# Optimization experiments

Hardware: AMD Instinct MI355X
Metric: run time of the kernel (lower is better)

## Reference

```python
import jax, jax.numpy as jnp
import numpy as np

N_HEADS = 16


def _rope(q, k, freq_cos, freq_sin):
    # q,k: [B,S,H,hd]; freqs: [S, hd//2]
    B, S, H, hd = q.shape
    qr, qi = q.reshape(B, S, H, hd // 2, 2)[..., 0], q.reshape(B, S, H, hd // 2, 2)[..., 1]
    kr, ki = k.reshape(B, S, H, hd // 2, 2)[..., 0], k.reshape(B, S, H, hd // 2, 2)[..., 1]
    fc = freq_cos[None, :, None, :]  # [1,S,1,hd//2]
    fs = freq_sin[None, :, None, :]
    q_out = jnp.stack([qr * fc - qi * fs, qr * fs + qi * fc], axis=-1).reshape(B, S, H, hd)
    k_out = jnp.stack([kr * fc - ki * fs, kr * fs + ki * fc], axis=-1).reshape(B, S, H, hd)
    return q_out, k_out


def setup_inputs() -> dict:
    key = jax.random.key(0)
    ks = jax.random.split(key, 7)
    B, S, D = 2, 2048, 2048
    hd = D // N_HEADS
    scale = 1.0 / np.sqrt(D)
    return {
        "x": jax.random.normal(ks[0], (B, S, D), dtype=jnp.float32),
        "freq_cos": jnp.cos(jax.random.normal(ks[1], (S, hd // 2), dtype=jnp.float32)),
        "freq_sin": jnp.sin(jax.random.normal(ks[2], (S, hd // 2), dtype=jnp.float32)),
        "wq": jax.random.normal(ks[3], (D, D), dtype=jnp.float32) * scale,
        "wk": jax.random.normal(ks[4], (D, D), dtype=jnp.float32) * scale,
        "wv": jax.random.normal(ks[5], (D, D), dtype=jnp.float32) * scale,
        "wo": jax.random.normal(ks[6], (D, D), dtype=jnp.float32) * scale,
    }


def reference(x, freq_cos, freq_sin, wq, wk, wv, wo):
    B, S, D = x.shape
    H = N_HEADS
    hd = D // H
    # torch nn.Linear(weight [out,in]): y = x @ W^T
    q = (x @ wq.T).reshape(B, S, H, hd)
    k = (x @ wk.T).reshape(B, S, H, hd)
    v = (x @ wv.T).reshape(B, S, H, hd)
    q, k = _rope(q, k, freq_cos, freq_sin)
    # [B,H,S,hd]
    q = q.transpose(0, 2, 1, 3)
    k = k.transpose(0, 2, 1, 3)
    v = v.transpose(0, 2, 1, 3)
    scores = jnp.einsum("bhqd,bhkd->bhqk", q, k) / jnp.sqrt(jnp.float32(hd))
    causal = jnp.triu(jnp.full((S, S), -jnp.inf, dtype=scores.dtype), k=1)
    scores = scores + causal[None, None, :, :]
    probs = jax.nn.softmax(scores, axis=-1)
    out = jnp.einsum("bhqk,bhkd->bhqd", probs, v)
    out = out.transpose(0, 2, 1, 3).reshape(B, S, D)
    return out @ wo.T
```

## Files before the change

kernel.cpp:

```cpp
#include <hip/hip_runtime.h>
#include <hip/hip_bf16.h>
#include <stdint.h>

typedef unsigned short u16;
typedef unsigned int   u32;

typedef __attribute__((ext_vector_type(8))) short bf16x8;
typedef __attribute__((ext_vector_type(4))) float f32x4;
typedef __attribute__((ext_vector_type(4))) float f4;
typedef __attribute__((ext_vector_type(4))) u16   u16x4;

#define GLOBAL_AS __attribute__((address_space(1)))
#define LDS_AS    __attribute__((address_space(3)))

#define QSCALE (0.088388347648318447f * 1.4426950408889634f)

__device__ __forceinline__ void gload_lds16(const void* gsrc, void* ldst) {
    __builtin_amdgcn_global_load_lds((GLOBAL_AS const u32*)gsrc,
                                     (LDS_AS u32*)ldst, 16, 0, 0);
}

__device__ __forceinline__ float b2f(u16 u) {
    union { u32 i; float f; } x; x.i = ((u32)u) << 16; return x.f;
}
__device__ __forceinline__ u16 f2b(float f) {
    u32 u = __builtin_bit_cast(u32, f);
    u = (u + 0x7fff + ((u >> 16) & 1)) >> 16;
    return (u16)u;
}
__device__ __forceinline__ u16 f2b_tr(float f) {
    return (u16)(__builtin_bit_cast(u32, f) >> 16);
}

__global__ __launch_bounds__(256) void f2bf_kernel(const float* __restrict__ in,
                                                   u16* __restrict__ out, int n4) {
    int i = blockIdx.x * blockDim.x + threadIdx.x;
    if (i >= n4) return;
    f4 v = ((const f4*)in)[i];
    u16x4 o;
    o[0] = f2b(v[0]); o[1] = f2b(v[1]); o[2] = f2b(v[2]); o[3] = f2b(v[3]);
    ((u16x4*)out)[i] = o;
}

__global__ __launch_bounds__(256) void rope_kernel(u16* __restrict__ qkv,
                                                   const float* __restrict__ fc,
                                                   const float* __restrict__ fs) {
    const int S = 2048;
    int idx = blockIdx.x * blockDim.x + threadIdx.x;
    const int p   = idx & 1023;
    const int row = idx >> 10;
    const int s   = row & (S - 1);
    const int i   = p & 63;
    const float c = fc[s * 64 + i], sn = fs[s * 64 + i];
    u16* qa = qkv + (size_t)row * 6144 + p * 2;
    u16* ka = qa + 2048;
    u32 qq = *(const u32*)qa;
    float qr = b2f((u16)(qq & 0xffff)), qi = b2f((u16)(qq >> 16));
    u32 kk = *(const u32*)ka;
    float kr = b2f((u16)(kk & 0xffff)), ki = b2f((u16)(kk >> 16));
    u16 e0 = f2b(qr * c - qi * sn), e1 = f2b(qr * sn + qi * c);
    *(u32*)qa = (u32)e0 | ((u32)e1 << 16);
    e0 = f2b(kr * c - ki * sn); e1 = f2b(kr * sn + ki * c);
    *(u32*)ka = (u32)e0 | ((u32)e1 << 16);
}

#define BARR() do { asm volatile("" ::: "memory"); \
                    __builtin_amdgcn_s_barrier();  \
                    asm volatile("" ::: "memory"); } while (0)

template<int OUT_MODE>
__global__ __launch_bounds__(512, 2)
void gemm8(const u16* __restrict__ A, const u16* __restrict__ B,
           void* __restrict__ Cptr, int M, int N, int Kdim) {
    __shared__ char lds[131072];
    const int t = threadIdx.x, l = t & 63, w = t >> 6;
    const int g = l >> 4, r16 = l & 15;
    const int wm = w >> 2, wn = w & 3;

    const int nwg = gridDim.x * gridDim.y;
    const int id  = blockIdx.y * gridDim.x + blockIdx.x;
    const int swz = (id & 7) * (nwg >> 3) + (id >> 3);
    const int bx  = swz % gridDim.x, by = swz / gridDim.x;
    const int m0 = by * 256, n0 = bx * 256;

    f32x4 acc[8][4];
#pragma unroll
    for (int i = 0; i < 8; i++)
#pragma unroll
        for (int j = 0; j < 4; j++) acc[i][j] = (f32x4){0.f, 0.f, 0.f, 0.f};

    const int sw  = (r16 & 7) << 4;
    const int cK0 = (g * 16) ^ sw;
    const int cK1 = (64 + g * 16) ^ sw;

    bf16x8 afA[4][2], bfA[2][2], bfB[2][2];

    auto stgA = [&](int d, int r, int kt) {
#pragma unroll
        for (int i = 0; i < 2; i++) {
            const int o  = (i * 8 + w) * 1024 + l * 16;
            const int rr = o >> 7;
            const int cb = (o & 127) ^ ((rr & 7) << 4);
            const int gr = ((rr >> 6) << 7) + r * 64 + (rr & 63);
            gload_lds16(A + (size_t)(m0 + gr) * Kdim + kt * 64 + (cb >> 1),
                        lds + d * 65536 + r * 16384 + (i * 8 + w) * 1024);
        }
    };
    auto stgB = [&](int d, int r, int kt) {
#pragma unroll
        for (int i = 0; i < 2; i++) {
            const int o  = (i * 8 + w) * 1024 + l * 16;
            const int rr = o >> 7;
            const int cb = (o & 127) ^ ((rr & 7) << 4);
            const int gc = ((rr >> 5) << 6) + r * 32 + (rr & 31);
            gload_lds16(B + (size_t)(n0 + gc) * Kdim + kt * 64 + (cb >> 1),
                        lds + d * 65536 + 32768 + r * 16384 + (i * 8 + w) * 1024);
        }
    };
    auto rdA = [&](int d, int qm) {
#pragma unroll
        for (int mi = 0; mi < 4; mi++) {
            const char* p = lds + d * 65536 + qm * 16384
                            + (wm * 64 + mi * 16 + r16) * 128;
            afA[mi][0] = *(const bf16x8*)(p + cK0);
            afA[mi][1] = *(const bf16x8*)(p + cK1);
        }
    };
    auto rdB = [&](bf16x8 (&dst)[2][2], int d, int qn) {
#pragma unroll
        for (int ni = 0; ni < 2; ni++) {
            const char* p = lds + d * 65536 + 32768 + qn * 16384
                            + (wn * 32 + ni * 16 + r16) * 128;
            dst[ni][0] = *(const bf16x8*)(p + cK0);
            dst[ni][1] = *(const bf16x8*)(p + cK1);
        }
    };
    auto mm = [&](int qm, int qn, bf16x8 (&bf)[2][2]) {
        __builtin_amdgcn_s_setprio(1);
#pragma unroll
        for (int kk = 0; kk < 2; kk++)
#pragma unroll
            for (int mi = 0; mi < 4; mi++)
#pragma unroll
                for (int ni = 0; ni < 2; ni++)
                    acc[qm * 4 + mi][qn * 2 + ni] =
                        __builtin_amdgcn_mfma_f32_16x16x32_bf16(
                            afA[mi][kk], bf[ni][kk],
                            acc[qm * 4 + mi][qn * 2 + ni], 0, 0, 0);
        __builtin_amdgcn_s_setprio(0);
    };

    const int nk = Kdim >> 6;

    stgA(0, 0, 0); stgB(0, 1, 0); stgB(0, 0, 0); stgA(0, 1, 0);
    stgA(1, 0, 1); stgB(1, 1, 1);
    asm volatile("s_waitcnt vmcnt(4)" ::: "memory");
    BARR();

    for (int tt = 0; tt < (nk >> 1); ++tt) {
        const int b1 = (2 * tt + 1);
        const int a2 = (2 * tt + 2) & (nk - 1);
        const int b2 = (2 * tt + 3) & (nk - 1);

        rdA(0, 0); rdB(bfA, 0, 0); stgB(1, 0, b1); BARR();
        mm(0, 0, bfA); BARR();
        rdB(bfB, 0, 1); stgA(1, 1, b1); BARR();
        mm(0, 1, bfB); BARR();
        rdA(0, 1); stgA(0, 0, a2); BARR();
        mm(1, 1, bfB); BARR();
        stgB(0, 1, a2); BARR();
        mm(1, 0, bfA);
        asm volatile("s_waitcnt vmcnt(4)" ::: "memory");
        BARR();
        rdA(1, 0); rdB(bfA, 1, 0); stgB(0, 0, a2); BARR();
        mm(0, 0, bfA); BARR();
        rdB(bfB, 1, 1); stgA(0, 1, a2); BARR();
        mm(0, 1, bfB); BARR();
        rdA(1, 1); stgA(1, 0, b2); BARR();
        mm(1, 1, bfB); BARR();
        stgB(1, 1, b2); BARR();
        mm(1, 0, bfA);
        asm volatile("s_waitcnt vmcnt(4)" ::: "memory");
        BARR();
    }

#pragma unroll
    for (int a = 0; a < 8; a++)
#pragma unroll
        for (int b = 0; b < 4; b++)
#pragma unroll
            for (int r = 0; r < 4; r++) {
                int row = m0 + wm * 128 + a * 16 + g * 4 + r;
                int col = n0 + wn * 64 + b * 16 + r16;
                float v = acc[a][b][r];
                if (OUT_MODE == 0)      ((float*)Cptr)[(size_t)row * N + col] = v;
                else if (OUT_MODE == 1) ((u16*)Cptr)[(size_t)row * N + col] = f2b(v);
                else ((u16*)Cptr)[(size_t)row * N + col] =
                         f2b(col < 2048 ? v * QSCALE : v);
            }
}

template<int OUT_MODE>
__global__ __launch_bounds__(512, 2)
void gemm_bt(const u16* __restrict__ A, const u16* __restrict__ B,
             void* __restrict__ Cptr, int M, int N, int Kdim) {
    __shared__ char lds[3][49152];
    const int t = threadIdx.x, l = t & 63, w = t >> 6;
    const int g = l >> 4, r16 = l & 15;

    const int nwg = gridDim.x * gridDim.y;
    const int id  = blockIdx.y * gridDim.x + blockIdx.x;
    const int swz = (id & 7) * (nwg >> 3) + (id >> 3);
    const int bx  = swz % gridDim.x, by = swz / gridDim.x;
    const int m0 = by * 256, n0 = bx * 128;
    const int wm = w >> 1, wn = w & 1;
    const int rA = wm * 64, rB = wn * 64;

    f32x4 acc[4][4];
#pragma unroll
    for (int i = 0; i < 4; i++)
#pragma unroll
        for (int j = 0; j < 4; j++) acc[i][j] = (f32x4){0.f, 0.f, 0.f, 0.f};

    const int nk = Kdim >> 6;

    auto stage = [&](int kt, int bi) {
        const int k0 = kt << 6;
#pragma unroll
        for (int q = 0; q < 4; q++) {
            const int o = q * 8192 + w * 1024 + l * 16;
            const int row = o >> 7;
            const int cb = (o & 127) ^ ((row & 7) << 4);
            gload_lds16(A + (size_t)(m0 + row) * Kdim + k0 + (cb >> 1),
                        &lds[bi][q * 8192 + w * 1024]);
        }
#pragma unroll
        for (int q = 0; q < 2; q++) {
            const int o = q * 8192 + w * 1024 + l * 16;
            const int row = o >> 7;
            const int cb = (o & 127) ^ ((row & 7) << 4);
            gload_lds16(B + (size_t)(n0 + row) * Kdim + k0 + (cb >> 1),
                        &lds[bi][32768 + q * 8192 + w * 1024]);
        }
    };

    stage(0, 0);
    stage(1, 1);

    for (int kt = 0; kt < nk; ++kt) {
        const int cur = kt % 3;
        __builtin_amdgcn_sched_barrier(0);
        __builtin_amdgcn_s_barrier();
        stage((kt + 2) % nk, (kt + 2) % 3);
        asm volatile("s_waitcnt vmcnt(12)" ::: "memory");
        __builtin_amdgcn_s_barrier();
        __builtin_amdgcn_sched_barrier(0);

        const char* Ab = lds[cur];
        const char* Bb = lds[cur] + 32768;
        bf16x8 af[2][4], bfr[2][4];
#pragma unroll
        for (int kk = 0; kk < 2; kk++)
#pragma unroll
            for (int i = 0; i < 4; i++) {
                const int rowa = rA + i * 16 + r16;
                const int cba = (kk * 64 + g * 16) ^ ((rowa & 7) << 4);
                af[kk][i] = *(const bf16x8*)(Ab + rowa * 128 + cba);
                const int rowb = rB + i * 16 + r16;
                const int cbb = (kk * 64 + g * 16) ^ ((rowb & 7) << 4);
                bfr[kk][i] = *(const bf16x8*)(Bb + rowb * 128 + cbb);
            }
#pragma unroll
        for (int kk = 0; kk < 2; kk++)
#pragma unroll
            for (int mi = 0; mi < 4; mi++)
#pragma unroll
                for (int ni = 0; ni < 4; ni++)
                    acc[mi][ni] = __builtin_amdgcn_mfma_f32_16x16x32_bf16(af[kk][mi],
                                                                          bfr[kk][ni],
                                                                          acc[mi][ni], 0, 0, 0);
    }

#pragma unroll
    for (int mi = 0; mi < 4; mi++)
#pragma unroll
        for (int ni = 0; ni < 4; ni++)
#pragma unroll
            for (int r = 0; r < 4; r++) {
                int row = m0 + rA + mi * 16 + g * 4 + r;
                int col = n0 + rB + ni * 16 + r16;
                float v = acc[mi][ni][r];
                if (OUT_MODE == 0)      ((float*)Cptr)[(size_t)row * N + col] = v;
                else if (OUT_MODE == 1) ((u16*)Cptr)[(size_t)row * N + col] = f2b(v);
                else ((u16*)Cptr)[(size_t)row * N + col] =
                         f2b(col < 2048 ? v * QSCALE : v);
            }
}

__global__ __launch_bounds__(512, 2)
void flash_attn(const u16* __restrict__ QKV, u16* __restrict__ Op) {
    const int S = 2048, DQ = 6144, DO = 2048;
    __shared__ u16 klds[2][128 * 128];
    __shared__ u16 vtlds[128 * 136];
    __shared__ u16 plds[8][16 * 136];
    const int t = threadIdx.x, l = t & 63, w = t >> 6;
    const int g = l >> 4, r16 = l & 15;
    const int bh = blockIdx.x, b = bh >> 4, h = bh & 15;
    const size_t base = ((size_t)(b * S)) * DQ + h * 128;
    const u16* qp = QKV + base;
    const u16* kp = qp + 2048;
    const u16* vp = qp + 4096;
    const size_t obase = ((size_t)(b * S)) * DO + h * 128;

    for (int task = 0; task < 2; ++task) {
        const int tq = task ? (15 - (int)blockIdx.y) : (int)blockIdx.y;
        const int q0 = tq * 128;
        const int nkt = tq + 1;

        bf16x8 qf[4];
#pragma unroll
        for (int ks = 0; ks < 4; ks++)
            qf[ks] = *(const bf16x8*)(qp + (size_t)(q0 + w * 16 + r16) * DQ
                                      + ks * 32 + g * 8);

        f32x4 acc[8];
#pragma unroll
        for (int i = 0; i < 8; i++) acc[i] = (f32x4){0.f, 0.f, 0.f, 0.f};
        float m_run[4], s_run[4];
#pragma unroll
        for (int r = 0; r < 4; r++) { m_run[r] = -3.0e38f; s_run[r] = 0.f; }

        auto stageK = [&](int bi, int kv0) {
#pragma unroll
            for (int i = 0; i < 4; i++) {
                const int o = (w * 4 + i) * 1024 + l * 16;
                const int row = o >> 8;
                const int cb = (o & 255) ^ ((row & 7) << 4);
                gload_lds16(kp + (size_t)(kv0 + row) * DQ + (cb >> 1),
                            (char*)klds[bi] + (w * 4 + i) * 1024);
            }
        };
        bf16x8 vv[2][2];
        auto loadV = [&](int kv0) {
#pragma unroll
            for (int c = 0; c < 2; c++)
#pragma unroll
                for (int kh = 0; kh < 2; kh++)
                    vv[c][kh] = *(const bf16x8*)(vp + (size_t)(kv0 + kh * 64 + l) * DQ
                                                 + (w * 16 + c * 8));
        };
        auto writeVT = [&]() {
#pragma unroll
            for (int c = 0; c < 2; c++)
#pragma unroll
                for (int kh = 0; kh < 2; kh++) {
                    const int d0 = w * 16 + c * 8;
#pragma unroll
                    for (int j = 0; j < 8; j++)
                        vtlds[(d0 + j) * 136 + kh * 64 + l] = (u16)vv[c][kh][j];
                }
        };

        stageK(0, 0);
        loadV(0);
        __syncthreads();
        writeVT();
        __syncthreads();

        int cur = 0;
        for (int kt = 0; kt < nkt; ++kt) {
            const int kv0 = kt * 128;
            const bool more = (kt + 1 < nkt);
            if (more) { stageK(cur ^ 1, kv0 + 128); loadV(kv0 + 128); }

            f32x4 sf[8];
#pragma unroll
            for (int nf = 0; nf < 8; nf++) sf[nf] = (f32x4){0.f, 0.f, 0.f, 0.f};
#pragma unroll
            for (int nf = 0; nf < 8; nf++) {
                const int row = nf * 16 + r16;
                const int rb = row * 256;
#pragma unroll
                for (int ks = 0; ks < 4; ks++) {
                    const int cb = (ks * 64 + g * 16) ^ ((row & 7) << 4);
                    bf16x8 kf = *(const bf16x8*)((const char*)klds[cur] + rb + cb);
                    sf[nf] = __builtin_amdgcn_mfma_f32_16x16x32_bf16(qf[ks], kf,
                                                                     sf[nf], 0, 0, 0);
                }
            }

            const bool diag = (kt == tq);
            float mt[4];
#pragma unroll
            for (int r = 0; r < 4; r++) mt[r] = -3.0e38f;
#pragma unroll
            for (int nf = 0; nf < 8; nf++)
#pragma unroll
                for (int r = 0; r < 4; r++) {
                    float s = sf[nf][r];
                    if (diag) {
                        int qrow = q0 + w * 16 + g * 4 + r;
                        int kcol = kv0 + nf * 16 + r16;
                        if (kcol > qrow) s = -3.0e38f;
                    }
                    sf[nf][r] = s;
                    mt[r] = fmaxf(mt[r], s);
                }
#pragma unroll
            for (int r = 0; r < 4; r++) {
#pragma unroll
                for (int d = 1; d < 16; d <<= 1)
                    mt[r] = fmaxf(mt[r], __shfl_xor(mt[r], d));
            }
            int grow = (mt[0] > m_run[0] + 8.f) | (mt[1] > m_run[1] + 8.f) |
                       (mt[2] > m_run[2] + 8.f) | (mt[3] > m_run[3] + 8.f);
            if (__any(grow)) {
#pragma unroll
                for (int r = 0; r < 4; r++) {
                    float mn = fmaxf(m_run[r], mt[r]);
                    float alpha = exp2f(m_run[r] - mn);
                    m_run[r] = mn;
                    s_run[r] *= alpha;
#pragma unroll
                    for (int i = 0; i < 8; i++) acc[i][r] *= alpha;
                }
            }
            float psum[4];
#pragma unroll
            for (int r = 0; r < 4; r++) psum[r] = 0.f;
#pragma unroll
            for (int nf = 0; nf < 8; nf++)
#pragma unroll
                for (int r = 0; r < 4; r++) {
                    float p = exp2f(sf[nf][r] - m_run[r]);
                    psum[r] += p;
                    plds[w][(g * 4 + r) * 136 + nf * 16 + r16] = f2b_tr(p);
                }
#pragma unroll
            for (int r = 0; r < 4; r++) {
#pragma unroll
                for (int d = 1; d < 16; d <<= 1)
                    psum[r] += __shfl_xor(psum[r], d);
                s_run[r] += psum[r];
            }
            __builtin_amdgcn_s_setprio(1);
#pragma unroll
            for (int ks2 = 0; ks2 < 4; ks2++) {
                bf16x8 pf = *(const bf16x8*)(&plds[w][r16 * 136 + ks2 * 32 + g * 8]);
#pragma unroll
                for (int nf8 = 0; nf8 < 8; nf8++) {
                    bf16x8 vf = *(const bf16x8*)(&vtlds[(nf8 * 16 + r16) * 136
                                                         + ks2 * 32 + g * 8]);
                    acc[nf8] = __builtin_amdgcn_mfma_f32_16x16x32_bf16(pf, vf,
                                                                       acc[nf8], 0, 0, 0);
                }
            }
            __builtin_amdgcn_s_setprio(0);

            __syncthreads();
            if (more) writeVT();
            __syncthreads();
            cur ^= 1;
        }

        float inv[4];
#pragma unroll
        for (int r = 0; r < 4; r++) inv[r] = 1.0f / s_run[r];
#pragma unroll
        for (int nf8 = 0; nf8 < 8; nf8++)
#pragma unroll
            for (int r = 0; r < 4; r++) {
                size_t idx = obase + (size_t)(q0 + w * 16 + g * 4 + r) * DO
                             + nf8 * 16 + r16;
                Op[idx] = f2b(acc[nf8][r] * inv[r]);
            }
    }
}

extern "C" void kernel_launch(void* const* d_in, const int* in_sizes, int n_in,
                              void* d_out, int out_size, void* d_ws, size_t ws_size,
                              hipStream_t stream) {
    const float* x  = (const float*)d_in[0];
    const float* fc = (const float*)d_in[1];
    const float* fs = (const float*)d_in[2];
    const float* wq = (const float*)d_in[3];
    const float* wk = (const float*)d_in[4];
    const float* wv = (const float*)d_in[5];
    const float* wo = (const float*)d_in[6];
    float* out = (float*)d_out;

    const int S = 2048, D = 2048;
    const int M = 2 * S;
    const size_t MD = (size_t)M * D;
    const size_t DD = (size_t)D * D;

    u16* xb   = (u16*)d_ws;
    u16* wqb  = xb  + MD;
    u16* wkb  = wqb + DD;
    u16* wvb  = wkb + DD;
    u16* wob  = wvb + DD;
    u16* qkvb = wob + DD;

    f2bf_kernel<<<(int)(MD / 1024), 256, 0, stream>>>(x,  xb,  (int)(MD / 4));
    f2bf_kernel<<<(int)(DD / 1024), 256, 0, stream>>>(wq, wqb, (int)(DD / 4));
    f2bf_kernel<<<(int)(DD / 1024), 256, 0, stream>>>(wk, wkb, (int)(DD / 4));
    f2bf_kernel<<<(int)(DD / 1024), 256, 0, stream>>>(wv, wvb, (int)(DD / 4));
    f2bf_kernel<<<(int)(DD / 1024), 256, 0, stream>>>(wo, wob, (int)(DD / 4));

    gemm8<2><<<dim3(6144 / 256, M / 256), 512, 0, stream>>>(xb, wqb, qkvb, M, 6144, D);

    rope_kernel<<<(int)(MD / 2 / 256), 256, 0, stream>>>(qkvb, fc, fs);

    flash_attn<<<dim3(32, 8), 512, 0, stream>>>(qkvb, xb);

    gemm_bt<0><<<dim3(D / 128, M / 256), 512, 0, stream>>>(xb, wob, out, M, D, D);
}
```

Before: 286.5 us.

## Fuse RoPE into QKV GEMM epilogue and merge fp32-to-bf16 casts

```diff
diff --git a/kernel.cpp b/kernel.cpp
--- a/kernel.cpp
+++ b/kernel.cpp
@@ -32,38 +32,27 @@
     return (u16)(__builtin_bit_cast(u32, f) >> 16);
 }
 
-__global__ __launch_bounds__(256) void f2bf_kernel(const float* __restrict__ in,
-                                                   u16* __restrict__ out, int n4) {
+__global__ __launch_bounds__(256)
+void f2bf_all(const float* __restrict__ x,  const float* __restrict__ wq,
+              const float* __restrict__ wk, const float* __restrict__ wv,
+              const float* __restrict__ wo, u16* __restrict__ out,
+              int md4, int dd4, int n4) {
     int i = blockIdx.x * blockDim.x + threadIdx.x;
     if (i >= n4) return;
-    f4 v = ((const f4*)in)[i];
+    const float* src; int off;
+    if (i < md4) { src = x; off = i; }
+    else {
+        int j = i - md4;
+        int k = j / dd4;
+        off = j - k * dd4;
+        src = (k == 0) ? wq : (k == 1) ? wk : (k == 2) ? wv : wo;
+    }
+    f4 v = ((const f4*)src)[off];
     u16x4 o;
     o[0] = f2b(v[0]); o[1] = f2b(v[1]); o[2] = f2b(v[2]); o[3] = f2b(v[3]);
     ((u16x4*)out)[i] = o;
 }
 
-__global__ __launch_bounds__(256) void rope_kernel(u16* __restrict__ qkv,
-                                                   const float* __restrict__ fc,
-                                                   const float* __restrict__ fs) {
-    const int S = 2048;
-    int idx = blockIdx.x * blockDim.x + threadIdx.x;
-    const int p   = idx & 1023;
-    const int row = idx >> 10;
-    const int s   = row & (S - 1);
-    const int i   = p & 63;
-    const float c = fc[s * 64 + i], sn = fs[s * 64 + i];
-    u16* qa = qkv + (size_t)row * 6144 + p * 2;
-    u16* ka = qa + 2048;
-    u32 qq = *(const u32*)qa;
-    float qr = b2f((u16)(qq & 0xffff)), qi = b2f((u16)(qq >> 16));
-    u32 kk = *(const u32*)ka;
-    float kr = b2f((u16)(kk & 0xffff)), ki = b2f((u16)(kk >> 16));
-    u16 e0 = f2b(qr * c - qi * sn), e1 = f2b(qr * sn + qi * c);
-    *(u32*)qa = (u32)e0 | ((u32)e1 << 16);
-    e0 = f2b(kr * c - ki * sn); e1 = f2b(kr * sn + ki * c);
-    *(u32*)ka = (u32)e0 | ((u32)e1 << 16);
-}
-
 #define BARR() do { asm volatile("" ::: "memory"); \
                     __builtin_amdgcn_s_barrier();  \
                     asm volatile("" ::: "memory"); } while (0)
@@ -71,7 +60,8 @@
 template<int OUT_MODE>
 __global__ __launch_bounds__(512, 2)
 void gemm8(const u16* __restrict__ A, const u16* __restrict__ B,
-           void* __restrict__ Cptr, int M, int N, int Kdim) {
+           void* __restrict__ Cptr, int M, int N, int Kdim,
+           const float* __restrict__ fc, const float* __restrict__ fs) {
     __shared__ char lds[131072];
     const int t = threadIdx.x, l = t & 63, w = t >> 6;
     const int g = l >> 4, r16 = l & 15;
@@ -193,10 +183,21 @@
                 int row = m0 + wm * 128 + a * 16 + g * 4 + r;
                 int col = n0 + wn * 64 + b * 16 + r16;
                 float v = acc[a][b][r];
-                if (OUT_MODE == 0)      ((float*)Cptr)[(size_t)row * N + col] = v;
-                else if (OUT_MODE == 1) ((u16*)Cptr)[(size_t)row * N + col] = f2b(v);
-                else ((u16*)Cptr)[(size_t)row * N + col] =
-                         f2b(col < 2048 ? v * QSCALE : v);
+                if (OUT_MODE == 0) {
+                    ((float*)Cptr)[(size_t)row * N + col] = v;
+                } else {
+                    float part = __shfl_xor(v, 1);
+                    float ov = v;
+                    if (col < 4096) {
+                        int s = row & 2047;
+                        int i = (col & 127) >> 1;
+                        float c  = fc[s * 64 + i];
+                        float sn = fs[s * 64 + i];
+                        ov = (col & 1) ? (part * sn + v * c) : (v * c - part * sn);
+                        if (col < 2048) ov *= QSCALE;
+                    }
+                    ((u16*)Cptr)[(size_t)row * N + col] = f2b(ov);
+                }
             }
 }
 
@@ -291,9 +292,7 @@
                 int col = n0 + rB + ni * 16 + r16;
                 float v = acc[mi][ni][r];
                 if (OUT_MODE == 0)      ((float*)Cptr)[(size_t)row * N + col] = v;
-                else if (OUT_MODE == 1) ((u16*)Cptr)[(size_t)row * N + col] = f2b(v);
-                else ((u16*)Cptr)[(size_t)row * N + col] =
-                         f2b(col < 2048 ? v * QSCALE : v);
+                else                    ((u16*)Cptr)[(size_t)row * N + col] = f2b(v);
             }
 }
 
@@ -496,20 +495,16 @@
 
     u16* xb   = (u16*)d_ws;
     u16* wqb  = xb  + MD;
-    u16* wkb  = wqb + DD;
-    u16* wvb  = wkb + DD;
-    u16* wob  = wvb + DD;
+    u16* wob  = wqb + 3 * DD;
     u16* qkvb = wob + DD;
 
-    f2bf_kernel<<<(int)(MD / 1024), 256, 0, stream>>>(x,  xb,  (int)(MD / 4));
-    f2bf_kernel<<<(int)(DD / 1024), 256, 0, stream>>>(wq, wqb, (int)(DD / 4));
-    f2bf_kernel<<<(int)(DD / 1024), 256, 0, stream>>>(wk, wkb, (int)(DD / 4));
-    f2bf_kernel<<<(int)(DD / 1024), 256, 0, stream>>>(wv, wvb, (int)(DD / 4));
-    f2bf_kernel<<<(int)(DD / 1024), 256, 0, stream>>>(wo, wob, (int)(DD / 4));
-
-    gemm8<2><<<dim3(6144 / 256, M / 256), 512, 0, stream>>>(xb, wqb, qkvb, M, 6144, D);
-
-    rope_kernel<<<(int)(MD / 2 / 256), 256, 0, stream>>>(qkvb, fc, fs);
+    const int md4 = (int)(MD / 4), dd4 = (int)(DD / 4);
+    const int n4  = md4 + 4 * dd4;
+    f2bf_all<<<(n4 + 255) / 256, 256, 0, stream>>>(x, wq, wk, wv, wo, xb,
+                                                   md4, dd4, n4);
+
+    gemm8<2><<<dim3(6144 / 256, M / 256), 512, 0, stream>>>(xb, wqb, qkvb,
+                                                            M, 6144, D, fc, fs);
 
     flash_attn<<<dim3(32, 8), 512, 0, stream>>>(qkvb, xb);
 
```

New measurement: 291.8 us. Within noise of the previous version (+1.8%).
